# Performance work log

Measured on AMD Instinct MI355X. Metric: run time of the kernel, lower is better.

## Reference

```python
import jax, jax.numpy as jnp
import numpy as np
from jax import lax

N = 32768      # points in the single input cloud
NIN = 16       # input per-point features
NH = 64        # nhidden
NOUT = 2
K = 32         # max_neighbors
DEPTH = 3
RADII = (2.0, 4.0, 8.0)
DIM = NH + 4   # PPFConv message dim: x_j (NH) + 4 point-pair features
CHUNK = 1024   # query chunk for brute-force radius search


def _fps(pos, n_samples):
    """Farthest point sampling, deterministic start at index 0 (eval mode)."""
    n = pos.shape[0]
    big = jnp.asarray(np.finfo(np.float32).max, pos.dtype)

    def body(carry, _):
        dists, last = carry
        d = jnp.sum((pos - pos[last]) ** 2, axis=-1)
        dists = jnp.minimum(dists, d)
        nxt = jnp.argmax(dists).astype(jnp.int32)
        return (dists, nxt), nxt

    init = (jnp.full((n,), big, pos.dtype), jnp.int32(0))
    _, rest = lax.scan(body, init, None, length=n_samples - 1)
    return jnp.concatenate([jnp.zeros((1,), jnp.int32), rest])


def _radius_knn(pos_q, pos, r, k):
    """For each query: indices of up to k points within radius r (+ validity mask).
    Chunked over queries so the [nq, n] distance matrix is never fully materialized."""
    nq = pos_q.shape[0]

    def f(qc):
        d2 = jnp.sum((qc[:, None, :] - pos[None, :, :]) ** 2, axis=-1)  # [CHUNK, n]
        neg_d2, idx = lax.top_k(-d2, k)
        valid = (-neg_d2) <= r * r
        return idx, valid

    idx, valid = lax.map(f, pos_q.reshape(-1, CHUNK, 3))
    return idx.reshape(nq, k), valid.reshape(nq, k)


def _angle(v1, v2):
    c = jnp.cross(v1, v2)
    return jnp.arctan2(jnp.linalg.norm(c, axis=-1), jnp.sum(v1 * v2, axis=-1))


def _ppf(pos_i, pos_j, n_i, n_j):
    d = pos_j - pos_i
    return jnp.stack([
        jnp.linalg.norm(d, axis=-1),
        _angle(n_i, d),
        _angle(n_j, d),
        _angle(n_i, n_j),
    ], axis=-1)


def _forward(x, pos, norm, lin_in_w0, lin_in_b0, lin_in_w1, lin_in_b1,
             sa_nn1_w0, sa_nn1_b0, sa_nn1_w1, sa_nn1_b1, sa_nn2_w, sa_nn2_b,
             lin_out_w0, lin_out_b0, lin_out_w1, lin_out_b1):
    # lin_in MLP
    h = jax.nn.relu(x @ lin_in_w0 + lin_in_b0)
    h = jax.nn.relu(h @ lin_in_w1 + lin_in_b1)

    cur_x, cur_pos, cur_norm = h, pos, norm
    for i in range(DEPTH):  # SAModules (structurally distinct levels)
        n_samples = cur_pos.shape[0] // 2  # ratio = 0.5
        idx = _fps(cur_pos, n_samples)
        pos_q = cur_pos[idx]
        norm_q = cur_norm[idx]
        nbr, valid = _radius_knn(pos_q, cur_pos, RADII[i], K)  # [nq, K]
        x_j = cur_x[nbr]                                       # [nq, K, NH]
        feats = _ppf(pos_q[:, None, :], cur_pos[nbr], norm_q[:, None, :], cur_norm[nbr])
        msg = jnp.concatenate([x_j, feats], axis=-1)           # [nq, K, DIM]
        # PPFConv local nn (nn1): Linear+ReLU x2
        m = jax.nn.relu(msg @ sa_nn1_w0[i] + sa_nn1_b0[i])
        m = jax.nn.relu(m @ sa_nn1_w1[i] + sa_nn1_b1[i])
        # max aggregation over valid neighbors (empty -> 0, matching torch_scatter)
        m = jnp.where(valid[..., None], m, -1e30)
        agg = jnp.max(m, axis=1)
        agg = jnp.where(valid.any(axis=1)[:, None], agg, 0.0)
        # PPFConv global nn (nn2): Linear+ReLU
        cur_x = jax.nn.relu(agg @ sa_nn2_w[i] + sa_nn2_b[i])
        cur_pos, cur_norm = pos_q, norm_q

    # global_mean_pool over the single graph -> [1, NH]
    pooled = jnp.mean(cur_x, axis=0, keepdims=True)
    o = jax.nn.relu(pooled @ lin_out_w0 + lin_out_b0)
    return o @ lin_out_w1 + lin_out_b1  # [1, NOUT]


_forward_jit = jax.jit(_forward)


def setup_inputs() -> dict:
    key = jax.random.key(0)
    ks = jax.random.split(key, 20)

    def w(k, *shape):
        return jax.random.normal(k, shape, jnp.float32) * float(np.sqrt(2.0 / shape[-2]))

    def b(k, *shape):
        return jax.random.normal(k, shape, jnp.float32) * 0.01

    x = jax.random.normal(ks[0], (N, NIN), jnp.float32)
    pos = jax.random.uniform(ks[1], (N, 3), dtype=jnp.float32) * 32.0  # unit density cube
    nrm = jax.random.normal(ks[2], (N, 3), jnp.float32)
    norm = nrm / jnp.linalg.norm(nrm, axis=-1, keepdims=True)

    return dict(
        x=x, pos=pos, norm=norm,
        lin_in_w0=w(ks[3], NIN, NH), lin_in_b0=b(ks[4], NH),
        lin_in_w1=w(ks[5], NH, NH), lin_in_b1=b(ks[6], NH),
        sa_nn1_w0=w(ks[7], DEPTH, DIM, DIM), sa_nn1_b0=b(ks[8], DEPTH, DIM),
        sa_nn1_w1=w(ks[9], DEPTH, DIM, DIM), sa_nn1_b1=b(ks[10], DEPTH, DIM),
        sa_nn2_w=w(ks[11], DEPTH, DIM, NH), sa_nn2_b=b(ks[12], DEPTH, NH),
        lin_out_w0=w(ks[13], NH, NH), lin_out_b0=b(ks[14], NH),
        lin_out_w1=w(ks[15], NH, NOUT), lin_out_b1=b(ks[16], NOUT),
    )


def reference(x, pos, norm, lin_in_w0, lin_in_b0, lin_in_w1, lin_in_b1,
              sa_nn1_w0, sa_nn1_b0, sa_nn1_w1, sa_nn1_b1, sa_nn2_w, sa_nn2_b,
              lin_out_w0, lin_out_b0, lin_out_w1, lin_out_b1):
    return _forward_jit(x, pos, norm, lin_in_w0, lin_in_b0, lin_in_w1, lin_in_b1,
                        sa_nn1_w0, sa_nn1_b0, sa_nn1_w1, sa_nn1_b1, sa_nn2_w, sa_nn2_b,
                        lin_out_w0, lin_out_b0, lin_out_w1, lin_out_b1)
```

## Files before the change

### kernel.cpp

```cpp
#include <hip/hip_runtime.h>
#include <math.h>

typedef unsigned long long u64;

#define TILE 2048
#define CAP 96
#define QB 32
#define NCELL 4096

__device__ __forceinline__ u64 wave_min_u64(u64 v) {
#pragma unroll
  for (int off = 32; off; off >>= 1) {
    u64 o = __shfl_xor(v, off, 64);
    v = (o < v) ? o : v;
  }
  return v;
}

__device__ __forceinline__ u64 wave_max_u64(u64 v) {
#pragma unroll
  for (int off = 32; off; off >>= 1) {
    u64 o = __shfl_xor(v, off, 64);
    v = (o > v) ? o : v;
  }
  return v;
}

__device__ __forceinline__ float angf(float ax, float ay, float az,
                                      float bx, float by, float bz) {
  float cx = ay * bz - az * by;
  float cy = az * bx - ax * bz;
  float cz = ax * by - ay * bx;
  float cn = sqrtf(cx * cx + cy * cy + cz * cz);
  float dt = ax * bx + ay * by + az * bz;
  return atan2f(cn, dt);
}

__device__ __forceinline__ int cell_of(float x, float y, float z) {
  int cx = (int)(x * 0.5f); cx = cx < 0 ? 0 : (cx > 15 ? 15 : cx);
  int cy = (int)(y * 0.5f); cy = cy < 0 ? 0 : (cy > 15 ? 15 : cy);
  int cz = (int)(z * 0.5f); cz = cz < 0 ? 0 : (cz > 15 ? 15 : cz);
  return (cz << 8) | (cy << 4) | cx;
}

__global__ __launch_bounds__(256) void k_lin_in(
    const float* __restrict__ x, const float* __restrict__ w0,
    const float* __restrict__ b0, const float* __restrict__ w1,
    const float* __restrict__ b1, float* __restrict__ h) {
  __shared__ __align__(16) float sW0[1024];
  __shared__ __align__(16) float sW1[4096];
  __shared__ float sB0[64], sB1[64];
  for (int i = threadIdx.x; i < 1024; i += 256) sW0[i] = w0[i];
  for (int i = threadIdx.x; i < 4096; i += 256) sW1[i] = w1[i];
  if (threadIdx.x < 64) { sB0[threadIdx.x] = b0[threadIdx.x]; sB1[threadIdx.x] = b1[threadIdx.x]; }
  __syncthreads();
  int p = blockIdx.x * 256 + threadIdx.x;
  float h1[64];
#pragma unroll
  for (int o = 0; o < 64; ++o) h1[o] = sB0[o];
#pragma unroll
  for (int c4 = 0; c4 < 4; ++c4) {
    float4 xv = *(const float4*)&x[p * 16 + 4 * c4];
#pragma unroll
    for (int u = 0; u < 4; ++u) {
      float v = (u == 0) ? xv.x : (u == 1) ? xv.y : (u == 2) ? xv.z : xv.w;
      int c = 4 * c4 + u;
#pragma unroll
      for (int o4 = 0; o4 < 16; ++o4) {
        float4 w = *(const float4*)&sW0[c * 64 + 4 * o4];
        h1[4 * o4 + 0] = fmaf(v, w.x, h1[4 * o4 + 0]);
        h1[4 * o4 + 1] = fmaf(v, w.y, h1[4 * o4 + 1]);
        h1[4 * o4 + 2] = fmaf(v, w.z, h1[4 * o4 + 2]);
        h1[4 * o4 + 3] = fmaf(v, w.w, h1[4 * o4 + 3]);
      }
    }
  }
#pragma unroll
  for (int o = 0; o < 64; ++o) h1[o] = fmaxf(h1[o], 0.f);
  float h2[64];
#pragma unroll
  for (int o = 0; o < 64; ++o) h2[o] = sB1[o];
#pragma unroll
  for (int c = 0; c < 64; ++c) {
    float v = h1[c];
#pragma unroll
    for (int o4 = 0; o4 < 16; ++o4) {
      float4 w = *(const float4*)&sW1[c * 64 + 4 * o4];
      h2[4 * o4 + 0] = fmaf(v, w.x, h2[4 * o4 + 0]);
      h2[4 * o4 + 1] = fmaf(v, w.y, h2[4 * o4 + 1]);
      h2[4 * o4 + 2] = fmaf(v, w.z, h2[4 * o4 + 2]);
      h2[4 * o4 + 3] = fmaf(v, w.w, h2[4 * o4 + 3]);
    }
  }
#pragma unroll
  for (int o4 = 0; o4 < 16; ++o4) {
    float4 o;
    o.x = fmaxf(h2[4 * o4 + 0], 0.f);
    o.y = fmaxf(h2[4 * o4 + 1], 0.f);
    o.z = fmaxf(h2[4 * o4 + 2], 0.f);
    o.w = fmaxf(h2[4 * o4 + 3], 0.f);
    *(float4*)&h[(long)p * 64 + 4 * o4] = o;
  }
}

__global__ __launch_bounds__(256) void k_precompA(
    const float* __restrict__ feat, const float* __restrict__ w,
    const float* __restrict__ b, float* __restrict__ A, int n) {
  __shared__ __align__(16) float sW[4352];
  __shared__ float sB[68];
  for (int i = threadIdx.x; i < 4352; i += 256) sW[i] = w[i];
  for (int i = threadIdx.x; i < 68; i += 256) sB[i] = b[i];
  __syncthreads();
  int p = blockIdx.x * 256 + threadIdx.x;
  if (p >= n) return;
  float acc[68];
#pragma unroll
  for (int o = 0; o < 68; ++o) acc[o] = sB[o];
#pragma unroll
  for (int c4 = 0; c4 < 16; ++c4) {
    float4 f = *(const float4*)&feat[(long)p * 64 + 4 * c4];
#pragma unroll
    for (int u = 0; u < 4; ++u) {
      float v = (u == 0) ? f.x : (u == 1) ? f.y : (u == 2) ? f.z : f.w;
      int c = 4 * c4 + u;
#pragma unroll
      for (int o4 = 0; o4 < 17; ++o4) {
        float4 wv = *(const float4*)&sW[c * 68 + 4 * o4];
        acc[4 * o4 + 0] = fmaf(v, wv.x, acc[4 * o4 + 0]);
        acc[4 * o4 + 1] = fmaf(v, wv.y, acc[4 * o4 + 1]);
        acc[4 * o4 + 2] = fmaf(v, wv.z, acc[4 * o4 + 2]);
        acc[4 * o4 + 3] = fmaf(v, wv.w, acc[4 * o4 + 3]);
      }
    }
  }
#pragma unroll
  for (int o4 = 0; o4 < 17; ++o4) {
    float4 o;
    o.x = acc[4 * o4 + 0]; o.y = acc[4 * o4 + 1];
    o.z = acc[4 * o4 + 2]; o.w = acc[4 * o4 + 3];
    *(float4*)&A[(long)p * 68 + 4 * o4] = o;
  }
}

__global__ __launch_bounds__(256) void k_zero_counts(int* __restrict__ c) {
  int i = blockIdx.x * 256 + threadIdx.x;
  if (i < NCELL) c[i] = 0;
}

__global__ __launch_bounds__(256) void k_hist(const float* __restrict__ pos,
                                              int n, int* __restrict__ counts) {
  int i = blockIdx.x * 256 + threadIdx.x;
  if (i >= n) return;
  atomicAdd(&counts[cell_of(pos[3 * i], pos[3 * i + 1], pos[3 * i + 2])], 1);
}

__global__ __launch_bounds__(512) void k_scan(const int* __restrict__ counts,
                                              int* __restrict__ starts,
                                              int* __restrict__ offs) {
  __shared__ int ps[512];
  int t = threadIdx.x;
  int loc[8], s = 0;
#pragma unroll
  for (int k = 0; k < 8; ++k) { loc[k] = counts[t * 8 + k]; s += loc[k]; }
  ps[t] = s;
  __syncthreads();
  for (int off = 1; off < 512; off <<= 1) {
    int v = (t >= off) ? ps[t - off] : 0;
    __syncthreads();
    ps[t] += v;
    __syncthreads();
  }
  int run = ps[t] - s;
#pragma unroll
  for (int k = 0; k < 8; ++k) {
    starts[t * 8 + k] = run;
    offs[t * 8 + k] = run;
    run += loc[k];
  }
  if (t == 511) starts[NCELL] = run;
}

__global__ __launch_bounds__(256) void k_scatter(
    const float* __restrict__ pos, int n, int* __restrict__ offs,
    float4* __restrict__ pts, int* __restrict__ sid, int* __restrict__ slot0) {
  int i = blockIdx.x * 256 + threadIdx.x;
  if (i >= n) return;
  float x = pos[3 * i], y = pos[3 * i + 1], z = pos[3 * i + 2];
  int c = cell_of(x, y, z);
  int slot = atomicAdd(&offs[c], 1);
  pts[slot] = make_float4(x, y, z, 3.402823466e38f);
  sid[slot] = i;
  if (i == 0) *slot0 = slot;
}

__global__ __launch_bounds__(512) void k_fps_cell(
    float4* __restrict__ pts, const int* __restrict__ sid,
    const int* __restrict__ starts, const int* __restrict__ slot0, int m,
    int* __restrict__ sel) {
#pragma clang fp contract(off)
  __shared__ u64 ck[NCELL];
  __shared__ int cs[NCELL + 1];
  __shared__ unsigned short sl[NCELL];
  __shared__ float bx[NCELL], by[NCELL], bz[NCELL];
  __shared__ int scnt[2];
  __shared__ u64 wk[2][8];
  const int t = threadIdx.x, lane = t & 63, wv = t >> 6;
  const u64 lmask = (1ull << lane) - 1ull;
  for (int c = t; c < NCELL + 1; c += 512) cs[c] = starts[c];
  __syncthreads();
  for (int c = t; c < NCELL; c += 512)
    ck[c] = (cs[c + 1] > cs[c]) ? ((u64)0x7F7FFFFFu << 27) : 0ull;
  if (t < 2) scnt[t] = 0;
  if (t == 0) sel[0] = 0;
  __syncthreads();
  float4 cp = pts[*slot0];
  float px = cp.x, py = cp.y, pz = cp.z;
  for (int i = 1; i < m; ++i) {
    const int par = i & 1;
    bool sv[8];
#pragma unroll
    for (int k = 0; k < 8; ++k) {
      int c = t + 512 * k;
      unsigned drmax = (unsigned)(ck[c] >> 27);
      float cx = (float)(((c & 15) << 1) + 1);
      float cy = (float)((((c >> 4) & 15) << 1) + 1);
      float cz = (float)(((c >> 8) << 1) + 1);
      float dx = fmaxf(fabsf(px - cx) - 1.f, 0.f);
      float dy = fmaxf(fabsf(py - cy) - 1.f, 0.f);
      float dz = fmaxf(fabsf(pz - cz) - 1.f, 0.f);
      float mind2 = (dx * dx + dy * dy) + dz * dz;
      sv[k] = __float_as_uint(mind2 * 0.9999f) < drmax;
    }
    u64 msk[8];
    int wtot = 0;
#pragma unroll
    for (int k = 0; k < 8; ++k) {
      msk[k] = __ballot(sv[k]);
      wtot += __popcll(msk[k]);
    }
    int wbase = 0;
    if (lane == 0 && wtot) wbase = atomicAdd(&scnt[par], wtot);
    wbase = __shfl(wbase, 0, 64);
#pragma unroll
    for (int k = 0; k < 8; ++k) {
      if (sv[k])
        sl[wbase + __popcll(msk[k] & lmask)] = (unsigned short)(t + 512 * k);
      wbase += __popcll(msk[k]);
    }
    if (t == 0) scnt[par ^ 1] = 0;
    __syncthreads();
    const int ns = scnt[par];
    const int g0 = t >> 3, l = t & 7;
    for (int g = g0; g < ns; g += 64) {
      int c = sl[g];
      int s = cs[c], e = cs[c + 1];
      u64 lk = 0;
      float lx = 0.f, ly = 0.f, lz = 0.f;
      for (int slot = s + l; slot < e; slot += 8) {
        float4 p = pts[slot];
        float ax = p.x - px, ay = p.y - py, az = p.z - pz;
        float d = (ax * ax + ay * ay) + az * az;
        float nd = fminf(p.w, d);
        ((float*)&pts[slot])[3] = nd;
        int o = sid[slot];
        u64 kk = ((u64)__float_as_uint(nd) << 27) |
                 ((u64)(unsigned)(32767 - o) << 12) | (unsigned)c;
        if (kk > lk) { lk = kk; lx = p.x; ly = p.y; lz = p.z; }
      }
#pragma unroll
      for (int off = 4; off; off >>= 1) {
        u64 ok = __shfl_xor(lk, off, 64);
        float ox = __shfl_xor(lx, off, 64);
        float oy = __shfl_xor(ly, off, 64);
        float oz = __shfl_xor(lz, off, 64);
        if (ok > lk) { lk = ok; lx = ox; ly = oy; lz = oz; }
      }
      if (l == 0) {
        ck[c] = lk; bx[c] = lx; by[c] = ly; bz[c] = lz;
      }
    }
    __syncthreads();
    u64 k = 0;
#pragma unroll
    for (int kk = 0; kk < 8; ++kk) {
      u64 v = ck[t + 512 * kk];
      if (v > k) k = v;
    }
    k = wave_max_u64(k);
    if (lane == 0) wk[par][wv] = k;
    __syncthreads();
    u64 best = wk[par][0];
#pragma unroll
    for (int w = 1; w < 8; ++w) {
      u64 v = wk[par][w];
      if (v > best) best = v;
    }
    int cell = (int)(best & 0xFFF);
    if (t == 0) sel[i] = 32767 - (int)((best >> 12) & 0x7FFF);
    px = bx[cell]; py = by[cell]; pz = bz[cell];
  }
}

__global__ __launch_bounds__(256) void k_gather(
    const float* __restrict__ pos, const float* __restrict__ nrm,
    const int* __restrict__ sel, int m, float* __restrict__ opos,
    float* __restrict__ onrm) {
  int i = blockIdx.x * 256 + threadIdx.x;
  if (i >= m) return;
  int s = sel[i];
  opos[3 * i + 0] = pos[3 * s + 0];
  opos[3 * i + 1] = pos[3 * s + 1];
  opos[3 * i + 2] = pos[3 * s + 2];
  onrm[3 * i + 0] = nrm[3 * s + 0];
  onrm[3 * i + 1] = nrm[3 * s + 1];
  onrm[3 * i + 2] = nrm[3 * s + 2];
}

__global__ __launch_bounds__(512) void k_conv(
    const float* __restrict__ qpos, const float* __restrict__ qnorm, int nq,
    const float* __restrict__ dpos, const float* __restrict__ dnorm, int n,
    const float* __restrict__ A, const float* __restrict__ w0p,
    const float* __restrict__ w1g, const float* __restrict__ b1g,
    const float* __restrict__ w2g, const float* __restrict__ b2g, float r2,
    float* __restrict__ xout) {
  __shared__ __align__(16) float smem[12288];
  __shared__ float aggS[QB][68];
  __shared__ int knnS[QB][32];
  __shared__ float qpS[QB][3], qnS[QB][3];
  __shared__ __align__(16) float w0pS[272];
  __shared__ float b1S[68], b2S[64];

  const int tid = threadIdx.x, lane = tid & 63, wv = tid >> 6;
  const int q0 = blockIdx.x * QB;
  float* tileS = smem;
  u64* cand = (u64*)&smem[6144];

  for (int i = tid; i < QB * 3; i += 512) {
    ((float*)qpS)[i] = qpos[q0 * 3 + i];
    ((float*)qnS)[i] = qnorm[q0 * 3 + i];
  }
  for (int i = tid; i < 272; i += 512) {
    int o = i >> 2, f = i & 3;
    w0pS[i] = w0p[f * 68 + o];
  }
  for (int i = tid; i < 68; i += 512) b1S[i] = b1g[i];
  for (int i = tid; i < 64; i += 512) b2S[i] = b2g[i];
  __syncthreads();

  float qx[4], qy[4], qz[4], thr[4];
  int cnt[4], tight[4];
#pragma unroll
  for (int qi = 0; qi < 4; ++qi) {
    int ql = wv * 4 + qi;
    qx[qi] = qpS[ql][0]; qy[qi] = qpS[ql][1]; qz[qi] = qpS[ql][2];
    thr[qi] = r2; cnt[qi] = 0; tight[qi] = 0;
  }
  const u64 lmask = (1ull << lane) - 1ull;
  for (int t0 = 0; t0 < n; t0 += TILE) {
    __syncthreads();
    for (int i = tid; i < TILE * 3; i += 512) tileS[i] = dpos[t0 * 3 + i];
    __syncthreads();
    for (int s = 0; s < TILE; s += 64) {
      int p = s + lane;
      float px = tileS[3 * p], py = tileS[3 * p + 1], pz = tileS[3 * p + 2];
      int gidx = t0 + p;
#pragma unroll
      for (int qi = 0; qi < 4; ++qi) {
        float d2;
        {
#pragma clang fp contract(off)
          float ax = px - qx[qi], ay = py - qy[qi], az = pz - qz[qi];
          d2 = (ax * ax + ay * ay) + az * az;
        }
        bool pred = tight[qi] ? (d2 < thr[qi]) : (d2 <= thr[qi]);
        u64 mask = __ballot(pred);
        if (mask) {
          int need = __popcll(mask);
          int base = (wv * 4 + qi) * CAP;
          if (cnt[qi] + need > CAP) {
            u64 v0 = (lane < cnt[qi]) ? cand[base + lane] : ~0ull;
            u64 v1 = (lane + 64 < cnt[qi]) ? cand[base + lane + 64] : ~0ull;
            u64 keep = ~0ull, last = 0;
            for (int it = 0; it < 32; ++it) {
              u64 mloc = (v0 < v1) ? v0 : v1;
              u64 mn = wave_min_u64(mloc);
              if (lane == it) keep = mn;
              if (v0 == mn) v0 = ~0ull; else if (v1 == mn) v1 = ~0ull;
              last = mn;
            }
            if (lane < 32) cand[base + lane] = keep;
            cnt[qi] = 32;
            thr[qi] = __uint_as_float((unsigned)(last >> 32));
            tight[qi] = 1;
          }
          if (pred) {
            int slot = cnt[qi] + __popcll(mask & lmask);
            cand[base + slot] = ((u64)__float_as_uint(d2) << 32) | (unsigned)gidx;
          }
          cnt[qi] += need;
        }
      }
    }
  }
#pragma unroll
  for (int qi = 0; qi < 4; ++qi) {
    int ql = wv * 4 + qi, base = ql * CAP, c = cnt[qi];
    int nout = (c < 32) ? c : 32;
    u64 v0 = (lane < c) ? cand[base + lane] : ~0ull;
    u64 v1 = (lane + 64 < c) ? cand[base + lane + 64] : ~0ull;
    int first = 0;
    for (int it = 0; it < 32; ++it) {
      u64 mloc = (v0 < v1) ? v0 : v1;
      u64 mn = wave_min_u64(mloc);
      int idx = (int)(mn & 0xffffffffu);
      if (it == 0) first = idx;
      int wr = (it < nout) ? idx : first;
      if (lane == it) knnS[ql][it] = wr;
      if (it < nout) {
        if (v0 == mn) v0 = ~0ull; else if (v1 == mn) v1 = ~0ull;
      }
    }
  }
  __syncthreads();
  for (int i = tid; i < 4624; i += 512) smem[i] = w1g[i];
  for (int i = tid; i < 4352; i += 512) smem[4624 + i] = w2g[i];
  __syncthreads();
  const float* W1s = smem;
  const float* W2s = smem + 4624;

#pragma unroll 1
  for (int r = 0; r < 2; ++r) {
    const int h = lane >> 5;
    const int ql = r * 16 + wv * 2 + h;
    const int kk = lane & 31;
    const int j = knnS[ql][kk];
    const float qx_ = qpS[ql][0], qy_ = qpS[ql][1], qz_ = qpS[ql][2];
    float dx = dpos[3 * j + 0] - qx_;
    float dy = dpos[3 * j + 1] - qy_;
    float dz = dpos[3 * j + 2] - qz_;
    float f0 = sqrtf(dx * dx + dy * dy + dz * dz);
    float nix = qnS[ql][0], niy = qnS[ql][1], niz = qnS[ql][2];
    float njx = dnorm[3 * j + 0], njy = dnorm[3 * j + 1], njz = dnorm[3 * j + 2];
    float f1 = angf(nix, niy, niz, dx, dy, dz);
    float f2 = angf(njx, njy, njz, dx, dy, dz);
    float f3 = angf(nix, niy, niz, njx, njy, njz);
    const float* Arow = A + (long)j * 68;
    float acc[68];
#pragma unroll
    for (int o = 0; o < 68; ++o) acc[o] = b1S[o];
    float4 a = *(const float4*)&Arow[0];
#pragma unroll 1
    for (int c4 = 0; c4 < 17; ++c4) {
      float4 an = (c4 < 16) ? *(const float4*)&Arow[4 * (c4 + 1)] : a;
#pragma unroll
      for (int u = 0; u < 4; ++u) {
        int c = 4 * c4 + u;
        float4 wf = *(const float4*)&w0pS[4 * c];
        float v = (u == 0) ? a.x : (u == 1) ? a.y : (u == 2) ? a.z : a.w;
        v = fmaf(f0, wf.x, v);
        v = fmaf(f1, wf.y, v);
        v = fmaf(f2, wf.z, v);
        v = fmaf(f3, wf.w, v);
        float mv = fmaxf(v, 0.f);
#pragma unroll
        for (int o4 = 0; o4 < 17; ++o4) {
          float4 wv4 = *(const float4*)&W1s[c * 68 + 4 * o4];
          acc[4 * o4 + 0] = fmaf(mv, wv4.x, acc[4 * o4 + 0]);
          acc[4 * o4 + 1] = fmaf(mv, wv4.y, acc[4 * o4 + 1]);
          acc[4 * o4 + 2] = fmaf(mv, wv4.z, acc[4 * o4 + 2]);
          acc[4 * o4 + 3] = fmaf(mv, wv4.w, acc[4 * o4 + 3]);
        }
      }
      a = an;
    }
#pragma unroll
    for (int o = 0; o < 68; ++o) {
      float v = fmaxf(acc[o], 0.f);
#pragma unroll
      for (int off = 16; off; off >>= 1) v = fmaxf(v, __shfl_xor(v, off, 64));
      if (kk == 0) aggS[ql][o] = v;
    }
  }
  __syncthreads();
  {
    const int ql = tid >> 4;
    const int og = (tid & 15) * 4;
    float a0 = b2S[og + 0], a1 = b2S[og + 1], a2 = b2S[og + 2], a3 = b2S[og + 3];
#pragma unroll
    for (int c = 0; c < 68; ++c) {
      float av = aggS[ql][c];
      float4 wv4 = *(const float4*)&W2s[c * 64 + og];
      a0 = fmaf(av, wv4.x, a0);
      a1 = fmaf(av, wv4.y, a1);
      a2 = fmaf(av, wv4.z, a2);
      a3 = fmaf(av, wv4.w, a3);
    }
    float4 o;
    o.x = fmaxf(a0, 0.f); o.y = fmaxf(a1, 0.f);
    o.z = fmaxf(a2, 0.f); o.w = fmaxf(a3, 0.f);
    *(float4*)&xout[(long)(q0 + ql) * 64 + og] = o;
  }
}

__global__ __launch_bounds__(256) void k_final(
    const float* __restrict__ x3, const float* __restrict__ w0,
    const float* __restrict__ b0, const float* __restrict__ w1,
    const float* __restrict__ b1, float* __restrict__ out) {
  __shared__ float part[4][64];
  __shared__ float pooled[64];
  __shared__ float hS[64];
  int t = threadIdx.x, c = t & 63, g = t >> 6;
  float s = 0.f;
  for (int i = g; i < 4096; i += 4) s += x3[(long)i * 64 + c];
  part[g][c] = s;
  __syncthreads();
  if (t < 64)
    pooled[t] = (part[0][t] + part[1][t] + part[2][t] + part[3][t]) * (1.f / 4096.f);
  __syncthreads();
  if (t < 64) {
    float a = b0[t];
    for (int cc = 0; cc < 64; ++cc) a = fmaf(pooled[cc], w0[cc * 64 + t], a);
    hS[t] = fmaxf(a, 0.f);
  }
  __syncthreads();
  if (t < 2) {
    float a = b1[t];
    for (int cc = 0; cc < 64; ++cc) a = fmaf(hS[cc], w1[cc * 2 + t], a);
    out[t] = a;
  }
}

extern "C" void kernel_launch(void* const* d_in, const int* in_sizes, int n_in,
                              void* d_out, int out_size, void* d_ws,
                              size_t ws_size, hipStream_t stream) {
  (void)in_sizes; (void)n_in; (void)out_size;
  const float* x     = (const float*)d_in[0];
  const float* pos   = (const float*)d_in[1];
  const float* nrm   = (const float*)d_in[2];
  const float* li_w0 = (const float*)d_in[3];
  const float* li_b0 = (const float*)d_in[4];
  const float* li_w1 = (const float*)d_in[5];
  const float* li_b1 = (const float*)d_in[6];
  const float* n1w0  = (const float*)d_in[7];
  const float* n1b0  = (const float*)d_in[8];
  const float* n1w1  = (const float*)d_in[9];
  const float* n1b1  = (const float*)d_in[10];
  const float* n2w   = (const float*)d_in[11];
  const float* n2b   = (const float*)d_in[12];
  const float* lo_w0 = (const float*)d_in[13];
  const float* lo_b0 = (const float*)d_in[14];
  const float* lo_w1 = (const float*)d_in[15];
  const float* lo_b1 = (const float*)d_in[16];
  float* out = (float*)d_out;

  char* ws = (char*)d_ws;
  size_t off = 0;
  auto alloc = [&](size_t nb) -> void* {
    void* p = (void*)(ws + off);
    off += nb;
    off = (off + 1023) & ~((size_t)1023);
    return p;
  };
  float* h     = (float*)alloc((size_t)32768 * 64 * 4);
  float* A0    = (float*)alloc((size_t)32768 * 68 * 4);
  int* counts  = (int*)  alloc((size_t)NCELL * 4);
  int* starts  = (int*)  alloc((size_t)(NCELL + 1) * 4);
  int* offs    = (int*)  alloc((size_t)NCELL * 4);
  float4* pts  = (float4*)alloc((size_t)32768 * 16);
  int* sid     = (int*)  alloc((size_t)32768 * 4);
  int* slot0   = (int*)  alloc((size_t)64);
  int*   sel0  = (int*)  alloc((size_t)16384 * 4);
  float* pos1  = (float*)alloc((size_t)16384 * 3 * 4);
  float* nrm1  = (float*)alloc((size_t)16384 * 3 * 4);
  float* x1    = (float*)alloc((size_t)16384 * 64 * 4);
  float* A1    = (float*)alloc((size_t)16384 * 68 * 4);
  int*   sel1  = (int*)  alloc((size_t)8192 * 4);
  float* pos2  = (float*)alloc((size_t)8192 * 3 * 4);
  float* nrm2  = (float*)alloc((size_t)8192 * 3 * 4);
  float* x2    = (float*)alloc((size_t)8192 * 64 * 4);
  float* A2    = (float*)alloc((size_t)8192 * 68 * 4);
  int*   sel2  = (int*)  alloc((size_t)4096 * 4);
  float* pos3  = (float*)alloc((size_t)4096 * 3 * 4);
  float* nrm3  = (float*)alloc((size_t)4096 * 3 * 4);
  float* x3    = (float*)alloc((size_t)4096 * 64 * 4);
  if (off > ws_size) return;

  k_lin_in<<<128, 256, 0, stream>>>(x, li_w0, li_b0, li_w1, li_b1, h);
  k_precompA<<<128, 256, 0, stream>>>(h, n1w0, n1b0, A0, 32768);

  k_zero_counts<<<16, 256, 0, stream>>>(counts);
  k_hist<<<128, 256, 0, stream>>>(pos, 32768, counts);
  k_scan<<<1, 512, 0, stream>>>(counts, starts, offs);
  k_scatter<<<128, 256, 0, stream>>>(pos, 32768, offs, pts, sid, slot0);
  k_fps_cell<<<1, 512, 0, stream>>>(pts, sid, starts, slot0, 16384, sel0);
  k_gather<<<64, 256, 0, stream>>>(pos, nrm, sel0, 16384, pos1, nrm1);
  k_conv<<<512, 512, 0, stream>>>(pos1, nrm1, 16384, pos, nrm, 32768, A0,
                                  n1w0 + 64 * 68, n1w1, n1b1, n2w, n2b, 4.0f,
                                  x1);

  k_zero_counts<<<16, 256, 0, stream>>>(counts);
  k_hist<<<64, 256, 0, stream>>>(pos1, 16384, counts);
  k_scan<<<1, 512, 0, stream>>>(counts, starts, offs);
  k_scatter<<<64, 256, 0, stream>>>(pos1, 16384, offs, pts, sid, slot0);
  k_fps_cell<<<1, 512, 0, stream>>>(pts, sid, starts, slot0, 8192, sel1);
  k_gather<<<32, 256, 0, stream>>>(pos1, nrm1, sel1, 8192, pos2, nrm2);
  k_precompA<<<64, 256, 0, stream>>>(x1, n1w0 + 68 * 68, n1b0 + 68, A1, 16384);
  k_conv<<<256, 512, 0, stream>>>(pos2, nrm2, 8192, pos1, nrm1, 16384, A1,
                                  n1w0 + 68 * 68 + 64 * 68, n1w1 + 68 * 68,
                                  n1b1 + 68, n2w + 68 * 64, n2b + 64, 16.0f,
                                  x2);

  k_zero_counts<<<16, 256, 0, stream>>>(counts);
  k_hist<<<32, 256, 0, stream>>>(pos2, 8192, counts);
  k_scan<<<1, 512, 0, stream>>>(counts, starts, offs);
  k_scatter<<<32, 256, 0, stream>>>(pos2, 8192, offs, pts, sid, slot0);
  k_fps_cell<<<1, 512, 0, stream>>>(pts, sid, starts, slot0, 4096, sel2);
  k_gather<<<16, 256, 0, stream>>>(pos2, nrm2, sel2, 4096, pos3, nrm3);
  k_precompA<<<32, 256, 0, stream>>>(x2, n1w0 + 2 * 68 * 68, n1b0 + 2 * 68, A2,
                                     8192);
  k_conv<<<128, 512, 0, stream>>>(pos3, nrm3, 4096, pos2, nrm2, 8192, A2,
                                  n1w0 + 2 * 68 * 68 + 64 * 68,
                                  n1w1 + 2 * 68 * 68, n1b1 + 2 * 68,
                                  n2w + 2 * 68 * 64, n2b + 2 * 64, 64.0f, x3);
  k_final<<<1, 256, 0, stream>>>(x3, lo_w0, lo_b0, lo_w1, lo_b1, out);
}
```

Baseline: 56.73 ms.

## Add two-level supercell hierarchy to FPS cell pruning with per-thread cached maxima

Cells are renumbered so each 2x2x2 group of cells forms a contiguous supercell owned by one thread. Each thread first tests its supercell's bounding box against its cached max distance key and only checks the eight child cells when that test passes. The per-cell key maxima are rescanned only when the thread touched a cell in this iteration, and a wave-level scan now replaces the ballot-based compaction. The distance field in the key moves to the high 32 bits so the pruning test can read it directly. The aim is to cut the per-iteration work of cell culling and max reduction in the serial FPS loop, at the cost of an extra prefix scan and more complex indexing.

```diff
diff --git a/kernel.cpp b/kernel.cpp
--- a/kernel.cpp
+++ b/kernel.cpp
@@ -40,7 +40,9 @@
   int cx = (int)(x * 0.5f); cx = cx < 0 ? 0 : (cx > 15 ? 15 : cx);
   int cy = (int)(y * 0.5f); cy = cy < 0 ? 0 : (cy > 15 ? 15 : cy);
   int cz = (int)(z * 0.5f); cz = cz < 0 ? 0 : (cz > 15 ? 15 : cz);
-  return (cz << 8) | (cy << 4) | cx;
+  int s = ((cz >> 1) << 6) | ((cy >> 1) << 3) | (cx >> 1);
+  int m = ((cz & 1) << 2) | ((cy & 1) << 1) | (cx & 1);
+  return s * 8 + m;
 }
 
 __global__ __launch_bounds__(256) void k_lin_in(
@@ -205,11 +207,22 @@
   __shared__ int scnt[2];
   __shared__ u64 wk[2][8];
   const int t = threadIdx.x, lane = t & 63, wv = t >> 6;
-  const u64 lmask = (1ull << lane) - 1ull;
+  const unsigned* ckhi = (const unsigned*)ck;
   for (int c = t; c < NCELL + 1; c += 512) cs[c] = starts[c];
   __syncthreads();
+  bool anyocc = false;
+#pragma unroll
+  for (int mm = 0; mm < 8; ++mm) {
+    int c = t * 8 + mm;
+    bool occ = cs[c + 1] > cs[c];
+    anyocc |= occ;
+  }
   for (int c = t; c < NCELL; c += 512)
-    ck[c] = (cs[c + 1] > cs[c]) ? ((u64)0x7F7FFFFFu << 27) : 0ull;
+    ck[c] = (cs[c + 1] > cs[c]) ? ((u64)0x7F7FFFFFu << 32) : 0ull;
+  u64 skreg = anyocc ? ((u64)0x7F7FFFFFu << 32) : 0ull;
+  const float scx = (float)((t & 7) * 4 + 2);
+  const float scy = (float)(((t >> 3) & 7) * 4 + 2);
+  const float scz = (float)(((t >> 6) & 7) * 4 + 2);
   if (t < 2) scnt[t] = 0;
   if (t == 0) sel[0] = 0;
   __syncthreads();
@@ -217,36 +230,48 @@
   float px = cp.x, py = cp.y, pz = cp.z;
   for (int i = 1; i < m; ++i) {
     const int par = i & 1;
+    int myns = 0;
     bool sv[8];
-#pragma unroll
-    for (int k = 0; k < 8; ++k) {
-      int c = t + 512 * k;
-      unsigned drmax = (unsigned)(ck[c] >> 27);
-      float cx = (float)(((c & 15) << 1) + 1);
-      float cy = (float)((((c >> 4) & 15) << 1) + 1);
-      float cz = (float)(((c >> 8) << 1) + 1);
-      float dx = fmaxf(fabsf(px - cx) - 1.f, 0.f);
-      float dy = fmaxf(fabsf(py - cy) - 1.f, 0.f);
-      float dz = fmaxf(fabsf(pz - cz) - 1.f, 0.f);
-      float mind2 = (dx * dx + dy * dy) + dz * dz;
-      sv[k] = __float_as_uint(mind2 * 0.9999f) < drmax;
-    }
-    u64 msk[8];
-    int wtot = 0;
-#pragma unroll
-    for (int k = 0; k < 8; ++k) {
-      msk[k] = __ballot(sv[k]);
-      wtot += __popcll(msk[k]);
-    }
-    int wbase = 0;
-    if (lane == 0 && wtot) wbase = atomicAdd(&scnt[par], wtot);
-    wbase = __shfl(wbase, 0, 64);
-#pragma unroll
-    for (int k = 0; k < 8; ++k) {
-      if (sv[k])
-        sl[wbase + __popcll(msk[k] & lmask)] = (unsigned short)(t + 512 * k);
-      wbase += __popcll(msk[k]);
-    }
+    {
+      float dx = fmaxf(fabsf(px - scx) - 2.f, 0.f);
+      float dy = fmaxf(fabsf(py - scy) - 2.f, 0.f);
+      float dz = fmaxf(fabsf(pz - scz) - 2.f, 0.f);
+      float mind2s = (dx * dx + dy * dy) + dz * dz;
+      bool ssv = __float_as_uint(mind2s * 0.9999f) < (unsigned)(skreg >> 32);
+#pragma unroll
+      for (int mm = 0; mm < 8; ++mm) sv[mm] = false;
+      if (ssv) {
+#pragma unroll
+        for (int mm = 0; mm < 8; ++mm) {
+          int c = t * 8 + mm;
+          float cx = scx + ((mm & 1) ? 1.f : -1.f);
+          float cy = scy + ((mm & 2) ? 1.f : -1.f);
+          float cz = scz + ((mm & 4) ? 1.f : -1.f);
+          float ex = fmaxf(fabsf(px - cx) - 1.f, 0.f);
+          float ey = fmaxf(fabsf(py - cy) - 1.f, 0.f);
+          float ez = fmaxf(fabsf(pz - cz) - 1.f, 0.f);
+          float mind2 = (ex * ex + ey * ey) + ez * ez;
+          bool s = __float_as_uint(mind2 * 0.9999f) < ckhi[2 * c + 1];
+          sv[mm] = s;
+          myns += s;
+        }
+      }
+    }
+    int pre = myns;
+#pragma unroll
+    for (int off = 1; off < 64; off <<= 1) {
+      int o = __shfl_up(pre, off, 64);
+      if (lane >= off) pre += o;
+    }
+    int wtot = __shfl(pre, 63, 64);
+    int excl = pre - myns;
+    int base = 0;
+    if (lane == 0 && wtot) base = atomicAdd(&scnt[par], wtot);
+    base = __shfl(base, 0, 64);
+    int slotw = base + excl;
+#pragma unroll
+    for (int mm = 0; mm < 8; ++mm)
+      if (sv[mm]) sl[slotw++] = (unsigned short)(t * 8 + mm);
     if (t == 0) scnt[par ^ 1] = 0;
     __syncthreads();
     const int ns = scnt[par];
@@ -263,7 +288,7 @@
         float nd = fminf(p.w, d);
         ((float*)&pts[slot])[3] = nd;
         int o = sid[slot];
-        u64 kk = ((u64)__float_as_uint(nd) << 27) |
+        u64 kk = ((u64)__float_as_uint(nd) << 32) |
                  ((u64)(unsigned)(32767 - o) << 12) | (unsigned)c;
         if (kk > lk) { lk = kk; lx = p.x; ly = p.y; lz = p.z; }
       }
@@ -280,13 +305,16 @@
       }
     }
     __syncthreads();
-    u64 k = 0;
-#pragma unroll
-    for (int kk = 0; kk < 8; ++kk) {
-      u64 v = ck[t + 512 * kk];
-      if (v > k) k = v;
-    }
-    k = wave_max_u64(k);
+    if (myns) {
+      u64 sk = 0;
+#pragma unroll
+      for (int mm = 0; mm < 8; ++mm) {
+        u64 v = ck[t * 8 + mm];
+        if (v > sk) sk = v;
+      }
+      skreg = sk;
+    }
+    u64 k = wave_max_u64(skreg);
     if (lane == 0) wk[par][wv] = k;
     __syncthreads();
     u64 best = wk[par][0];
```

Result: slower. 64.10 ms (+13.0%).

## Use register-resident brute-force FPS for the last level and realign cell keys

Applied to the files above, without the earlier changes.

For the third sampling level (8192 points), the cell-grid FPS plus its histogram, scan and scatter kernels are replaced by a single-block brute-force FPS. It keeps x, y and running min-distances in registers and z in shared memory, and finds the argmax with a wave shuffle followed by a cross-wave reduction. The cell FPS key now places the distance at bit 32, so the upper half can be read as a 32-bit word instead of shifting a 64-bit value. The aim is to drop the overhead of cell bookkeeping and four launches where the point count is small enough that scanning every point is cheap, at the cost of touching all points on every iteration.

```diff
diff --git a/kernel.cpp b/kernel.cpp
--- a/kernel.cpp
+++ b/kernel.cpp
@@ -206,10 +206,11 @@
   __shared__ u64 wk[2][8];
   const int t = threadIdx.x, lane = t & 63, wv = t >> 6;
   const u64 lmask = (1ull << lane) - 1ull;
+  const unsigned* ckhi = (const unsigned*)ck;
   for (int c = t; c < NCELL + 1; c += 512) cs[c] = starts[c];
   __syncthreads();
   for (int c = t; c < NCELL; c += 512)
-    ck[c] = (cs[c + 1] > cs[c]) ? ((u64)0x7F7FFFFFu << 27) : 0ull;
+    ck[c] = (cs[c + 1] > cs[c]) ? ((u64)0x7F7FFFFFu << 32) : 0ull;
   if (t < 2) scnt[t] = 0;
   if (t == 0) sel[0] = 0;
   __syncthreads();
@@ -221,7 +222,7 @@
 #pragma unroll
     for (int k = 0; k < 8; ++k) {
       int c = t + 512 * k;
-      unsigned drmax = (unsigned)(ck[c] >> 27);
+      unsigned drmax = ckhi[2 * c + 1];
       float cx = (float)(((c & 15) << 1) + 1);
       float cy = (float)((((c >> 4) & 15) << 1) + 1);
       float cz = (float)(((c >> 8) << 1) + 1);
@@ -263,7 +264,7 @@
         float nd = fminf(p.w, d);
         ((float*)&pts[slot])[3] = nd;
         int o = sid[slot];
-        u64 kk = ((u64)__float_as_uint(nd) << 27) |
+        u64 kk = ((u64)__float_as_uint(nd) << 32) |
                  ((u64)(unsigned)(32767 - o) << 12) | (unsigned)c;
         if (kk > lk) { lk = kk; lx = p.x; ly = p.y; lz = p.z; }
       }
@@ -298,6 +299,59 @@
     int cell = (int)(best & 0xFFF);
     if (t == 0) sel[i] = 32767 - (int)((best >> 12) & 0x7FFF);
     px = bx[cell]; py = by[cell]; pz = bz[cell];
+  }
+}
+
+template <int P>
+__global__ __launch_bounds__(512) void k_fps_breg(
+    const float* __restrict__ pos, int n, int m, int* __restrict__ sel) {
+#pragma clang fp contract(off)
+  __shared__ float zb[512 * P];
+  __shared__ u64 wk[2][8];
+  const int t = threadIdx.x, lane = t & 63, wv = t >> 6;
+  float xr[P], yr[P], dr[P];
+#pragma unroll
+  for (int j = 0; j < P; ++j) {
+    int idx = t + 512 * j;
+    xr[j] = pos[3 * idx + 0];
+    yr[j] = pos[3 * idx + 1];
+    zb[idx] = pos[3 * idx + 2];
+    dr[j] = 3.402823466e38f;
+  }
+  if (t == 0) sel[0] = 0;
+  __syncthreads();
+  int cur = 0;
+  for (int i = 1; i < m; ++i) {
+    float px = pos[3 * cur + 0], py = pos[3 * cur + 1], pz = pos[3 * cur + 2];
+    float bv = -1.f;
+    int bi = 0;
+#pragma unroll
+    for (int j = 0; j < P; ++j) {
+      int idx = t + 512 * j;
+      float ax = xr[j] - px, ay = yr[j] - py, az = zb[idx] - pz;
+      float d = (ax * ax + ay * ay) + az * az;
+      float nd = fminf(dr[j], d);
+      dr[j] = nd;
+      if (nd > bv) { bv = nd; bi = idx; }
+    }
+#pragma unroll
+    for (int off = 32; off; off >>= 1) {
+      float ov = __shfl_xor(bv, off, 64);
+      int oi = __shfl_xor(bi, off, 64);
+      if (ov > bv || (ov == bv && oi < bi)) { bv = ov; bi = oi; }
+    }
+    int par = i & 1;
+    if (lane == 0)
+      wk[par][wv] = ((u64)__float_as_uint(bv) << 32) | (unsigned)(~bi);
+    __syncthreads();
+    u64 bk = wk[par][0];
+#pragma unroll
+    for (int w = 1; w < 8; ++w) {
+      u64 o = wk[par][w];
+      if (o > bk) bk = o;
+    }
+    cur = (int)(~(unsigned)bk);
+    if (t == 0) sel[i] = cur;
   }
 }
 
@@ -610,11 +664,7 @@
                                   n1b1 + 68, n2w + 68 * 64, n2b + 64, 16.0f,
                                   x2);
 
-  k_zero_counts<<<16, 256, 0, stream>>>(counts);
-  k_hist<<<32, 256, 0, stream>>>(pos2, 8192, counts);
-  k_scan<<<1, 512, 0, stream>>>(counts, starts, offs);
-  k_scatter<<<32, 256, 0, stream>>>(pos2, 8192, offs, pts, sid, slot0);
-  k_fps_cell<<<1, 512, 0, stream>>>(pts, sid, starts, slot0, 4096, sel2);
+  k_fps_breg<16><<<1, 512, 0, stream>>>(pos2, 8192, 4096, sel2);
   k_gather<<<16, 256, 0, stream>>>(pos2, nrm2, sel2, 4096, pos3, nrm3);
   k_precompA<<<32, 256, 0, stream>>>(x2, n1w0 + 2 * 68 * 68, n1b0 + 2 * 68, A2,
                                      8192);
```

Measured after the change: 54.12 ms. 4.6% less time.
